# Kernel optimization log

Hardware: AMD Instinct MI355X
Metric: run time of the kernel (lower is better)

## Reference

```python
import jax, jax.numpy as jnp
import numpy as np

NEG = -1e9
BN_EPS = 1e-3  # keras BatchNormalization default epsilon
LRELU = 0.2    # GAT leaky-relu slope


def _gat(Xt, bias_mat, Wg, a1, a2, bg):
    """Dense multi-head GAT (Velickovic TF impl).
    Xt: [B,N,F], bias_mat: [B,N,N] additive mask (0 / -1e9).
    Wg: [H,F,D], a1/a2/bg: [H,D]. Returns [B,N,H*D]."""
    feats = jnp.einsum('bnf,hfd->bhnd', Xt, Wg)          # [B,H,N,D]
    f1 = jnp.einsum('bhnd,hd->bhn', feats, a1)
    f2 = jnp.einsum('bhnd,hd->bhn', feats, a2)
    logits = f1[:, :, :, None] + f2[:, :, None, :]        # [B,H,N,N]
    logits = jax.nn.leaky_relu(logits, LRELU) + bias_mat[:, None]
    coefs = jax.nn.softmax(logits, axis=-1)
    vals = jnp.einsum('bhnm,bhmd->bhnd', coefs, feats) + bg[None, :, None, :]
    vals = jax.nn.elu(vals)
    B, H, N, D = vals.shape
    return jnp.transpose(vals, (0, 2, 1, 3)).reshape(B, N, H * D)


def setup_inputs() -> dict:
    key = jax.random.key(0)
    ks = jax.random.split(key, 16)
    B, T, N, F = 4, 12, 2048, 64
    H, D = 4, 16           # attn_heads, hid_units
    C = H * D              # out_channels = 64

    X = jax.random.normal(ks[0], (B, T, N, F), dtype=jnp.float32)
    # random sparse adjacency (~avg degree 16) + self loops -> additive mask
    adj = jax.random.uniform(ks[1], (B, N, N)) < (16.0 / N)
    adj = adj | jnp.eye(N, dtype=bool)[None]
    bias_mat = jnp.where(adj, 0.0, NEG).astype(jnp.float32)

    he = lambda k, s: jax.random.normal(k, s, dtype=jnp.float32) * np.sqrt(2.0 / s[-2] if len(s) > 1 else 2.0 / s[-1])
    return {
        'X': X, 'bias_mat': bias_mat,
        'W_z': he(ks[2], (F, C)), 'Z_bias': he(ks[3], (1, C)),
        'W_h': he(ks[4], (F, C)), 'H_bias': he(ks[5], (1, C)),
        'Wg_z': he(ks[6], (H, F, D)), 'a1_z': he(ks[7], (H, D)),
        'a2_z': he(ks[8], (H, D)), 'bg_z': jnp.zeros((H, D), jnp.float32),
        'Wg_h': he(ks[9], (H, F, D)), 'a1_h': he(ks[10], (H, D)),
        'a2_h': he(ks[11], (H, D)), 'bg_h': jnp.zeros((H, D), jnp.float32),
        'bn_gamma': jnp.ones((C,), jnp.float32), 'bn_beta': jnp.zeros((C,), jnp.float32),
        'bn_mean': jnp.zeros((C,), jnp.float32), 'bn_var': jnp.ones((C,), jnp.float32),
    }


def reference(X, bias_mat, W_z, Z_bias, W_h, H_bias,
              Wg_z, a1_z, a2_z, bg_z, Wg_h, a1_h, a2_h, bg_h,
              bn_gamma, bn_beta, bn_mean, bn_var):
    B, T, N, F = X.shape
    C = W_z.shape[1]
    H0 = jnp.zeros((B, N, C), dtype=jnp.float32)

    def step(Hc, Xt):
        Z = _gat(Xt, bias_mat, Wg_z, a1_z, a2_z, bg_z) + Xt @ W_z + Z_bias + Hc
        Z = jax.nn.sigmoid(Z)
        Tt = _gat(Xt, bias_mat, Wg_h, a1_h, a2_h, bg_h) + Hc + Xt @ W_h + H_bias
        Tt = jnp.tanh(Tt)
        Hn = Z * Hc + (1.0 - Z) * Tt
        return Hn, None

    Xs = jnp.transpose(X, (1, 0, 2, 3))  # [T,B,N,F]
    Hf, _ = jax.lax.scan(step, H0, Xs)
    # last_layer=True path: BatchNorm (inference, moving stats) on final H
    out = (Hf - bn_mean) * jax.lax.rsqrt(bn_var + BN_EPS) * bn_gamma + bn_beta
    return out
```

## Files before the change

### kernel.cpp

```cpp
#include <hip/hip_runtime.h>
#include <cstdint>
#include <cstddef>

#define NB 4
#define NT 12
#define NN 2048
#define NF 64
#define NH 4
#define ND 16
#define NC 64
#define MAXD 64
#define NR (NB * NT * NN)

typedef _Float16 f16x8 __attribute__((ext_vector_type(8)));
typedef _Float16 f16x2 __attribute__((ext_vector_type(2)));
typedef float f32x4 __attribute__((ext_vector_type(4)));

#define LR(v) ((v) >= 0.f ? (v) : 0.2f * (v))
#define RCPF(x) __builtin_amdgcn_rcpf(x)

__global__ __launch_bounds__(256) void build_adj_k(const float* __restrict__ bias,
                                                   int* __restrict__ adj,
                                                   int* __restrict__ deg) {
  int gtid = blockIdx.x * 256 + threadIdx.x;
  int wid = gtid >> 6;
  int lane = threadIdx.x & 63;
  if (wid >= NB * NN) return;
  const float* row = bias + (size_t)wid * NN;
  int* arow = adj + (size_t)wid * MAXD;
  int count = 0;
  for (int c0 = 0; c0 < NN; c0 += 64) {
    float v = __builtin_nontemporal_load(row + c0 + lane);
    bool e = (v > -1e8f);
    unsigned long long m = __ballot(e);
    int pre = __popcll(m & ((1ull << lane) - 1ull));
    if (e) {
      int pos = count + pre;
      if (pos < MAXD) arow[pos] = c0 + lane;
    }
    count += __popcll(m);
  }
  if (lane == 0) deg[wid] = count < MAXD ? count : MAXD;
}

__global__ __launch_bounds__(256) void prep_w_k(
    const float* __restrict__ Wgz, const float* __restrict__ Wgh,
    const float* __restrict__ Wz,  const float* __restrict__ Wh,
    const float* __restrict__ a1z, const float* __restrict__ a2z,
    const float* __restrict__ a1h, const float* __restrict__ a2h,
    const float* __restrict__ Zb,  const float* __restrict__ Hb,
    _Float16* __restrict__ W16, float* __restrict__ biasC) {
  int idx = blockIdx.x * 256 + threadIdx.x;
  if (idx < 272 * 64) {
    int c = idx >> 6, k = idx & 63;
    float w;
    if (c < 64)       w = Wgz[((c >> 4) << 10) + (k << 4) + (c & 15)];
    else if (c < 128) { int q = c - 64; w = Wgh[((q >> 4) << 10) + (k << 4) + (q & 15)]; }
    else if (c < 192) w = Wz[(k << 6) + (c - 128)];
    else if (c < 256) w = Wh[(k << 6) + (c - 192)];
    else {
      int j = c - 256, h = j & 3;
      const float* Wg = (j & 4) ? Wgh : Wgz;
      const float* av = (j & 8) ? ((j & 4) ? a2h : a2z) : ((j & 4) ? a1h : a1z);
      float s = 0.f;
#pragma unroll
      for (int d = 0; d < 16; d++)
        s = fmaf(Wg[(h << 10) + (k << 4) + d], av[(h << 4) + d], s);
      w = s;
    }
    W16[idx] = (_Float16)w;
  }
  if (blockIdx.x == 0 && threadIdx.x < 128)
    biasC[threadIdx.x] =
        (threadIdx.x < 64) ? Zb[threadIdx.x] : Hb[threadIdx.x - 64];
}

__global__ __launch_bounds__(256) void mfma_gemm_k(
    const float* __restrict__ X, const _Float16* __restrict__ W16,
    const float* __restrict__ biasC,
    uint32_t* __restrict__ gbufF, uint32_t* __restrict__ gbufS,
    float* __restrict__ fbuf) {
  const int tid = threadIdx.x;
  const int wv = tid >> 6, lane = tid & 63;
  const int m = lane & 15, quad = lane >> 4;
  const unsigned rw = blockIdx.x * 64 + wv * 16;

  const float* xr = X + (size_t)(rw + m) * 64;
  float4 x0 = *(const float4*)(xr + quad * 8);
  float4 x1 = *(const float4*)(xr + quad * 8 + 4);
  float4 x2 = *(const float4*)(xr + 32 + quad * 8);
  float4 x3 = *(const float4*)(xr + 32 + quad * 8 + 4);
  f16x8 A0 = {(_Float16)x0.x, (_Float16)x0.y, (_Float16)x0.z, (_Float16)x0.w,
              (_Float16)x1.x, (_Float16)x1.y, (_Float16)x1.z, (_Float16)x1.w};
  f16x8 A1 = {(_Float16)x2.x, (_Float16)x2.y, (_Float16)x2.z, (_Float16)x2.w,
              (_Float16)x3.x, (_Float16)x3.y, (_Float16)x3.z, (_Float16)x3.w};

  float bzc[4], bhc[4];
#pragma unroll
  for (int j = 0; j < 4; j++) {
    bzc[j] = biasC[j * 16 + m];
    bhc[j] = biasC[64 + j * 16 + m];
  }

  f32x4 zacc[4], zs[4];
#pragma unroll
  for (int ct = 0; ct < 17; ct++) {
    const _Float16* wp = W16 + (ct * 16 + m) * 64;
    f16x8 B0 = *(const f16x8*)(wp + quad * 8);
    f16x8 B1 = *(const f16x8*)(wp + 32 + quad * 8);
    f32x4 acc = {0.f, 0.f, 0.f, 0.f};
    acc = __builtin_amdgcn_mfma_f32_16x16x32_f16(A0, B0, acc, 0, 0, 0);
    acc = __builtin_amdgcn_mfma_f32_16x16x32_f16(A1, B1, acc, 0, 0, 0);
    const unsigned rb = rw + quad * 4;
    if (ct < 4) {
      zacc[ct] = acc;
    } else if (ct < 8) {
      const int chn = (ct - 4) * 16 + m;
#pragma unroll
      for (int r = 0; r < 4; r++) {
        f16x2 pv = {(_Float16)zacc[ct - 4][r], (_Float16)acc[r]};
        gbufF[(rb + r) * 64 + chn] = __builtin_bit_cast(uint32_t, pv);
      }
    } else if (ct < 12) {
#pragma unroll
      for (int r = 0; r < 4; r++) zs[ct - 8][r] = acc[r] + bzc[ct - 8];
    } else if (ct < 16) {
      const int chn = (ct - 12) * 16 + m;
#pragma unroll
      for (int r = 0; r < 4; r++) {
        f16x2 pv = {(_Float16)zs[ct - 12][r], (_Float16)(acc[r] + bhc[ct - 12])};
        gbufS[(rb + r) * 64 + chn] = __builtin_bit_cast(uint32_t, pv);
      }
    } else {
#pragma unroll
      for (int r = 0; r < 4; r++) fbuf[(size_t)(rb + r) * 16 + m] = acc[r];
    }
  }
}

__global__ __launch_bounds__(256) void attn_k(
    const uint32_t* __restrict__ gbufF, const uint32_t* __restrict__ gbufS,
    const float* __restrict__ fbuf,
    const int* __restrict__ adj, const int* __restrict__ deg,
    const float* __restrict__ bgz, const float* __restrict__ bgh,
    float2* __restrict__ abuf) {
  __shared__ int adjL[MAXD];
  __shared__ float wexp[4][8][68];
  const int tid = threadIdx.x;
  const int lane = tid & 63;
  const int ws = tid >> 6;
  const int node = blockIdx.y;
  const int t = blockIdx.x * 4 + ws;
  const int b = node >> 11;
  const int nl = node & (NN - 1);
  const int dg = deg[node];
  if (tid < MAXD) adjL[tid] = (tid < dg) ? adj[node * MAXD + tid] : 0;
  __syncthreads();
  const int dgp = (dg + 7) & ~7;

  const unsigned rb = (unsigned)(b * NT + t) * NN;
  const float* fb = fbuf + (size_t)rb * 16;
  const uint32_t* gF = gbufF + (size_t)rb * 64;
  const uint32_t* gS = gbufS + (size_t)rb * 64;
  const int ch = lane, hh = lane >> 4;

  {
    const float4* p = (const float4*)(fb + nl * 16);
    int mm = adjL[lane];
    const float4* q = (const float4*)(fb + mm * 16);
    float4 f1z = p[0], f1h = p[1], f2z = q[2], f2h = q[3];
    bool act = lane < dg;
    wexp[ws][0][lane] = act ? __expf(LR(f1z.x + f2z.x)) : 0.f;
    wexp[ws][1][lane] = act ? __expf(LR(f1z.y + f2z.y)) : 0.f;
    wexp[ws][2][lane] = act ? __expf(LR(f1z.z + f2z.z)) : 0.f;
    wexp[ws][3][lane] = act ? __expf(LR(f1z.w + f2z.w)) : 0.f;
    wexp[ws][4][lane] = act ? __expf(LR(f1h.x + f2h.x)) : 0.f;
    wexp[ws][5][lane] = act ? __expf(LR(f1h.y + f2h.y)) : 0.f;
    wexp[ws][6][lane] = act ? __expf(LR(f1h.z + f2h.z)) : 0.f;
    wexp[ws][7][lane] = act ? __expf(LR(f1h.w + f2h.w)) : 0.f;
  }

  float az = 0.f, ah = 0.f, sz = 0.f, sh = 0.f;
  const float* wz = wexp[ws][hh];
  const float* wh = wexp[ws][4 + hh];
  for (int mi = 0; mi < dgp; mi += 8) {
    int4 ma = *(const int4*)&adjL[mi];
    int4 mb = *(const int4*)&adjL[mi + 4];
    float4 wza = *(const float4*)&wz[mi];
    float4 wzb = *(const float4*)&wz[mi + 4];
    float4 wha = *(const float4*)&wh[mi];
    float4 whb = *(const float4*)&wh[mi + 4];
    uint32_t d0 = gF[(ma.x << 6) + ch];
    uint32_t d1 = gF[(ma.y << 6) + ch];
    uint32_t d2 = gF[(ma.z << 6) + ch];
    uint32_t d3 = gF[(ma.w << 6) + ch];
    uint32_t d4 = gF[(mb.x << 6) + ch];
    uint32_t d5 = gF[(mb.y << 6) + ch];
    uint32_t d6 = gF[(mb.z << 6) + ch];
    uint32_t d7 = gF[(mb.w << 6) + ch];
    f16x2 p0 = __builtin_bit_cast(f16x2, d0);
    f16x2 p1 = __builtin_bit_cast(f16x2, d1);
    f16x2 p2 = __builtin_bit_cast(f16x2, d2);
    f16x2 p3 = __builtin_bit_cast(f16x2, d3);
    f16x2 p4 = __builtin_bit_cast(f16x2, d4);
    f16x2 p5 = __builtin_bit_cast(f16x2, d5);
    f16x2 p6 = __builtin_bit_cast(f16x2, d6);
    f16x2 p7 = __builtin_bit_cast(f16x2, d7);
    az = fmaf(wza.x, (float)p0.x, az); ah = fmaf(wha.x, (float)p0.y, ah);
    az = fmaf(wza.y, (float)p1.x, az); ah = fmaf(wha.y, (float)p1.y, ah);
    az = fmaf(wza.z, (float)p2.x, az); ah = fmaf(wha.z, (float)p2.y, ah);
    az = fmaf(wza.w, (float)p3.x, az); ah = fmaf(wha.w, (float)p3.y, ah);
    az = fmaf(wzb.x, (float)p4.x, az); ah = fmaf(whb.x, (float)p4.y, ah);
    az = fmaf(wzb.y, (float)p5.x, az); ah = fmaf(whb.y, (float)p5.y, ah);
    az = fmaf(wzb.z, (float)p6.x, az); ah = fmaf(whb.z, (float)p6.y, ah);
    az = fmaf(wzb.w, (float)p7.x, az); ah = fmaf(whb.w, (float)p7.y, ah);
    sz += (wza.x + wza.y) + (wza.z + wza.w) + (wzb.x + wzb.y) + (wzb.z + wzb.w);
    sh += (wha.x + wha.y) + (wha.z + wha.w) + (whb.x + whb.y) + (whb.z + whb.w);
  }
  az *= RCPF(sz);
  ah *= RCPF(sh);

  f16x2 sp = __builtin_bit_cast(f16x2, gS[(nl << 6) + ch]);
  float vz = az + bgz[ch]; vz = vz > 0.f ? vz : __expf(vz) - 1.f;
  float vh = ah + bgh[ch]; vh = vh > 0.f ? vh : __expf(vh) - 1.f;
  abuf[(size_t)(rb + nl) * 64 + ch] =
      make_float2(vz + (float)sp.x, vh + (float)sp.y);
}

__global__ __launch_bounds__(256) void gru_k(
    const float2* __restrict__ abuf,
    const float* __restrict__ gam, const float* __restrict__ bet,
    const float* __restrict__ mu, const float* __restrict__ var,
    float* __restrict__ out) {
  const int gtid = blockIdx.x * 256 + threadIdx.x;
  const int node = gtid >> 6, ch = gtid & 63;
  const int b = node >> 11, nl = node & (NN - 1);
  float hc = 0.f;
#pragma unroll
  for (int t = 0; t < NT; t++) {
    float2 pre = abuf[(size_t)((b * NT + t) * NN + nl) * 64 + ch];
    float zg = RCPF(1.f + __expf(-(pre.x + hc)));
    float ta = pre.y + hc;
    float tg = 1.f - 2.f * RCPF(__expf(2.f * ta) + 1.f);
    hc = zg * hc + (1.f - zg) * tg;
  }
  out[gtid] = (hc - mu[ch]) * rsqrtf(var[ch] + 1e-3f) * gam[ch] + bet[ch];
}

extern "C" void kernel_launch(void* const* d_in, const int* in_sizes, int n_in,
                              void* d_out, int out_size, void* d_ws, size_t ws_size,
                              hipStream_t stream) {
  (void)in_sizes; (void)n_in; (void)out_size; (void)ws_size;
  const float* X   = (const float*)d_in[0];
  const float* bm  = (const float*)d_in[1];
  const float* Wz  = (const float*)d_in[2];
  const float* Zb  = (const float*)d_in[3];
  const float* Wh  = (const float*)d_in[4];
  const float* Hb  = (const float*)d_in[5];
  const float* Wgz = (const float*)d_in[6];
  const float* a1z = (const float*)d_in[7];
  const float* a2z = (const float*)d_in[8];
  const float* bgz = (const float*)d_in[9];
  const float* Wgh = (const float*)d_in[10];
  const float* a1h = (const float*)d_in[11];
  const float* a2h = (const float*)d_in[12];
  const float* bgh = (const float*)d_in[13];
  const float* gam = (const float*)d_in[14];
  const float* bet = (const float*)d_in[15];
  const float* mu  = (const float*)d_in[16];
  const float* var = (const float*)d_in[17];
  float* out = (float*)d_out;

  char* p = (char*)d_ws;
  uint32_t* gbufF = (uint32_t*)p; p += (size_t)NR * 64 * sizeof(uint32_t);
  uint32_t* gbufS = (uint32_t*)p; p += (size_t)NR * 64 * sizeof(uint32_t);
  float*    fbuf  = (float*)p;    p += (size_t)NR * 16 * sizeof(float);
  float2*   abuf  = (float2*)p;   p += (size_t)NR * 64 * sizeof(float2);
  int*      adj   = (int*)p;      p += (size_t)NB * NN * MAXD * sizeof(int);
  int*      deg   = (int*)p;      p += (size_t)NB * NN * sizeof(int);
  _Float16* W16   = (_Float16*)p; p += 272 * 64 * sizeof(_Float16);
  float*    biasC = (float*)p;    p += 128 * sizeof(float);

  prep_w_k<<<dim3(68), dim3(256), 0, stream>>>(
      Wgz, Wgh, Wz, Wh, a1z, a2z, a1h, a2h, Zb, Hb, W16, biasC);
  build_adj_k<<<dim3(NB * NN / 4), dim3(256), 0, stream>>>(bm, adj, deg);
  mfma_gemm_k<<<dim3(NR / 64), dim3(256), 0, stream>>>(
      X, W16, biasC, gbufF, gbufS, fbuf);
  attn_k<<<dim3(NT / 4, NB * NN), dim3(256), 0, stream>>>(
      gbufF, gbufS, fbuf, adj, deg, bgz, bgh, abuf);
  gru_k<<<dim3(NB * NN * 64 / 256), dim3(256), 0, stream>>>(
      abuf, gam, bet, mu, var, out);
}
```

Measured before the change: 254.1 us.

## Stage GEMM outputs through LDS for coalesced stores; remap attention blocks

The MFMA GEMM kernel now writes its fp16-pair outputs into a per-wave LDS tile and then stores whole 16-byte rows to gbufF/gbufS, replacing scattered 4-byte stores. The attention kernel is remapped so each block handles four nodes at one timestep instead of one node across four timesteps. Each wave keeps its own adjacency list, which removes the block-wide barrier, and neighbour loads are skipped for inactive lanes. The LDS staging adds shared memory and relies on wave-local ordering with no explicit barrier. The new mapping changes gather locality, since the four waves in a block now read from the same timestep slice.

```diff
diff --git a/kernel.cpp b/kernel.cpp
--- a/kernel.cpp
+++ b/kernel.cpp
@@ -80,10 +80,12 @@
     const float* __restrict__ biasC,
     uint32_t* __restrict__ gbufF, uint32_t* __restrict__ gbufS,
     float* __restrict__ fbuf) {
+  __shared__ uint32_t tr[4][16 * 68];
   const int tid = threadIdx.x;
   const int wv = tid >> 6, lane = tid & 63;
   const int m = lane & 15, quad = lane >> 4;
   const unsigned rw = blockIdx.x * 64 + wv * 16;
+  uint32_t* tw = tr[wv];
 
   const float* xr = X + (size_t)(rw + m) * 64;
   float4 x0 = *(const float4*)(xr + quad * 8);
@@ -101,6 +103,7 @@
     bzc[j] = biasC[j * 16 + m];
     bhc[j] = biasC[64 + j * 16 + m];
   }
+  const int rsub = lane >> 4, chk = lane & 15;
 
   f32x4 zacc[4], zs[4];
 #pragma unroll
@@ -111,27 +114,43 @@
     f32x4 acc = {0.f, 0.f, 0.f, 0.f};
     acc = __builtin_amdgcn_mfma_f32_16x16x32_f16(A0, B0, acc, 0, 0, 0);
     acc = __builtin_amdgcn_mfma_f32_16x16x32_f16(A1, B1, acc, 0, 0, 0);
-    const unsigned rb = rw + quad * 4;
     if (ct < 4) {
       zacc[ct] = acc;
     } else if (ct < 8) {
-      const int chn = (ct - 4) * 16 + m;
+      const int j = ct - 4;
 #pragma unroll
       for (int r = 0; r < 4; r++) {
-        f16x2 pv = {(_Float16)zacc[ct - 4][r], (_Float16)acc[r]};
-        gbufF[(rb + r) * 64 + chn] = __builtin_bit_cast(uint32_t, pv);
+        f16x2 pv = {(_Float16)zacc[j][r], (_Float16)acc[r]};
+        tw[(quad * 4 + r) * 68 + j * 16 + m] = __builtin_bit_cast(uint32_t, pv);
+      }
+      if (ct == 7) {
+#pragma unroll
+        for (int i = 0; i < 4; i++) {
+          int row = i * 4 + rsub;
+          uint4 v = *(const uint4*)&tw[row * 68 + chk * 4];
+          *(uint4*)&gbufF[(size_t)(rw + row) * 64 + chk * 4] = v;
+        }
       }
     } else if (ct < 12) {
 #pragma unroll
       for (int r = 0; r < 4; r++) zs[ct - 8][r] = acc[r] + bzc[ct - 8];
     } else if (ct < 16) {
-      const int chn = (ct - 12) * 16 + m;
+      const int j = ct - 12;
 #pragma unroll
       for (int r = 0; r < 4; r++) {
-        f16x2 pv = {(_Float16)zs[ct - 12][r], (_Float16)(acc[r] + bhc[ct - 12])};
-        gbufS[(rb + r) * 64 + chn] = __builtin_bit_cast(uint32_t, pv);
+        f16x2 pv = {(_Float16)zs[j][r], (_Float16)(acc[r] + bhc[j])};
+        tw[(quad * 4 + r) * 68 + j * 16 + m] = __builtin_bit_cast(uint32_t, pv);
+      }
+      if (ct == 15) {
+#pragma unroll
+        for (int i = 0; i < 4; i++) {
+          int row = i * 4 + rsub;
+          uint4 v = *(const uint4*)&tw[row * 68 + chk * 4];
+          *(uint4*)&gbufS[(size_t)(rw + row) * 64 + chk * 4] = v;
+        }
       }
     } else {
+      const unsigned rb = rw + quad * 4;
 #pragma unroll
       for (int r = 0; r < 4; r++) fbuf[(size_t)(rb + r) * 16 + m] = acc[r];
     }
@@ -144,18 +163,17 @@
     const int* __restrict__ adj, const int* __restrict__ deg,
     const float* __restrict__ bgz, const float* __restrict__ bgh,
     float2* __restrict__ abuf) {
-  __shared__ int adjL[MAXD];
+  __shared__ int adjL[4][MAXD];
   __shared__ float wexp[4][8][68];
   const int tid = threadIdx.x;
   const int lane = tid & 63;
   const int ws = tid >> 6;
-  const int node = blockIdx.y;
-  const int t = blockIdx.x * 4 + ws;
+  const int node = blockIdx.x * 4 + ws;
+  const int t = blockIdx.y;
   const int b = node >> 11;
   const int nl = node & (NN - 1);
   const int dg = deg[node];
-  if (tid < MAXD) adjL[tid] = (tid < dg) ? adj[node * MAXD + tid] : 0;
-  __syncthreads();
+  adjL[ws][lane] = (lane < dg) ? adj[node * MAXD + lane] : 0;
   const int dgp = (dg + 7) & ~7;
 
   const unsigned rb = (unsigned)(b * NT + t) * NN;
@@ -166,26 +184,31 @@
 
   {
     const float4* p = (const float4*)(fb + nl * 16);
-    int mm = adjL[lane];
-    const float4* q = (const float4*)(fb + mm * 16);
-    float4 f1z = p[0], f1h = p[1], f2z = q[2], f2h = q[3];
-    bool act = lane < dg;
-    wexp[ws][0][lane] = act ? __expf(LR(f1z.x + f2z.x)) : 0.f;
-    wexp[ws][1][lane] = act ? __expf(LR(f1z.y + f2z.y)) : 0.f;
-    wexp[ws][2][lane] = act ? __expf(LR(f1z.z + f2z.z)) : 0.f;
-    wexp[ws][3][lane] = act ? __expf(LR(f1z.w + f2z.w)) : 0.f;
-    wexp[ws][4][lane] = act ? __expf(LR(f1h.x + f2h.x)) : 0.f;
-    wexp[ws][5][lane] = act ? __expf(LR(f1h.y + f2h.y)) : 0.f;
-    wexp[ws][6][lane] = act ? __expf(LR(f1h.z + f2h.z)) : 0.f;
-    wexp[ws][7][lane] = act ? __expf(LR(f1h.w + f2h.w)) : 0.f;
+    float4 f1z = p[0], f1h = p[1];
+    if (lane < dg) {
+      int mm = adjL[ws][lane];
+      const float4* q = (const float4*)(fb + mm * 16);
+      float4 f2z = q[2], f2h = q[3];
+      wexp[ws][0][lane] = __expf(LR(f1z.x + f2z.x));
+      wexp[ws][1][lane] = __expf(LR(f1z.y + f2z.y));
+      wexp[ws][2][lane] = __expf(LR(f1z.z + f2z.z));
+      wexp[ws][3][lane] = __expf(LR(f1z.w + f2z.w));
+      wexp[ws][4][lane] = __expf(LR(f1h.x + f2h.x));
+      wexp[ws][5][lane] = __expf(LR(f1h.y + f2h.y));
+      wexp[ws][6][lane] = __expf(LR(f1h.z + f2h.z));
+      wexp[ws][7][lane] = __expf(LR(f1h.w + f2h.w));
+    } else {
+#pragma unroll
+      for (int k = 0; k < 8; k++) wexp[ws][k][lane] = 0.f;
+    }
   }
 
   float az = 0.f, ah = 0.f, sz = 0.f, sh = 0.f;
   const float* wz = wexp[ws][hh];
   const float* wh = wexp[ws][4 + hh];
   for (int mi = 0; mi < dgp; mi += 8) {
-    int4 ma = *(const int4*)&adjL[mi];
-    int4 mb = *(const int4*)&adjL[mi + 4];
+    int4 ma = *(const int4*)&adjL[ws][mi];
+    int4 mb = *(const int4*)&adjL[ws][mi + 4];
     float4 wza = *(const float4*)&wz[mi];
     float4 wzb = *(const float4*)&wz[mi + 4];
     float4 wha = *(const float4*)&wh[mi];
@@ -286,7 +309,7 @@
   build_adj_k<<<dim3(NB * NN / 4), dim3(256), 0, stream>>>(bm, adj, deg);
   mfma_gemm_k<<<dim3(NR / 64), dim3(256), 0, stream>>>(
       X, W16, biasC, gbufF, gbufS, fbuf);
-  attn_k<<<dim3(NT / 4, NB * NN), dim3(256), 0, stream>>>(
+  attn_k<<<dim3(NB * NN / 4, NT), dim3(256), 0, stream>>>(
       gbufF, gbufS, fbuf, adj, deg, bgz, bgh, abuf);
   gru_k<<<dim3(NB * NN * 64 / 256), dim3(256), 0, stream>>>(
       abuf, gam, bet, mu, var, out);
```

Measured after the change: 250.1 us. Within noise of the previous version (-1.6%).
